# Optimization experiments

Measured on AMD Instinct MI355X. Metric: run time of the kernel, lower is better.

## Reference

```python
import jax, jax.numpy as jnp
import numpy as np

N, C, R, P1, P2 = 8, 3, 8, 512, 512
EPS = 1e-10


def setup_inputs() -> dict:
    key = jax.random.key(0)
    k1, k2, k3, k4 = jax.random.split(key, 4)
    X = jax.random.uniform(k1, (N, C, P1, P2), dtype=jnp.float32)
    S = jax.random.uniform(k2, (C, R), dtype=jnp.float32)
    # mimic the learned-init normalization: unit-norm columns of S
    S = S / jnp.linalg.norm(S, axis=0, keepdims=True)
    gamma = jax.random.uniform(k3, (1,), dtype=jnp.float32) * 1e-5
    lam = jax.random.uniform(k4, (1,), dtype=jnp.float32) * 1e-5
    return {"X": X, "S": S, "gamma": gamma, "lam": lam, "n_iter": 3}


def reference(X, S, gamma, lam, n_iter):
    n, c, p1, p2 = X.shape
    r = S.shape[1]
    p = p1 * p2
    X = X.reshape(n, c, p)
    gamma = jnp.abs(gamma)  # (1,)
    lam = jnp.abs(lam)      # (1,)
    Dt = jnp.zeros((n, r, p), dtype=X.dtype)
    x0 = jnp.mean(X, axis=2, keepdims=True)
    for _ in range(n_iter):
        # ---- D update (proximal gradient) ----
        SDt = jnp.einsum('cr,nrp->ncp', S, Dt)                    # [n,c,p]
        x0 = jnp.mean(X + SDt, axis=2, keepdims=True)             # [n,c,1]
        tau_D = 1.0 / jnp.sum(S * S)                              # 1/||S||_F^2
        Dt = Dt - tau_D * (jnp.einsum('cr,ncp->nrp', S, SDt + X)
                           - jnp.einsum('cr,ncq->nrq', S, x0))
        S_nrm = jnp.linalg.norm(S, axis=0).reshape(1, r, 1)       # col L2 norms of S
        Dt = jax.nn.relu(Dt - lam * gamma * tau_D * S_nrm)        # L1 prox
        Dt_L2 = jnp.linalg.norm(Dt, axis=2, keepdims=True)        # [n,r,1]
        scl = jax.nn.relu(Dt_L2 - lam * tau_D * S_nrm)
        scl = scl / Dt_L2 + EPS                                   # faithful to source
        Dt = Dt * scl                                             # L2 (group) prox
        # ---- S update (proximal gradient) ----
        SDt = jnp.einsum('cr,nrp->ncp', S, Dt)
        x0 = jnp.mean(X + SDt, axis=2, keepdims=True)             # [n,c,1]
        Dt_sum = jnp.sum(Dt, axis=2, keepdims=True)               # [n,r,1]
        tau_S = 1.0 / jnp.mean(jnp.sum(Dt * Dt, axis=(1, 2)))     # 1/mean ||Dt_i||_F^2
        G = (jnp.einsum('ncp,nrp->ncr', SDt + X, Dt)
             - x0 @ jnp.swapaxes(Dt_sum, 1, 2))                   # [n,c,r]
        S_grad = S - tau_S * jnp.mean(G, axis=0)                  # [c,r]
        Dt_nrm = jnp.mean(gamma * jnp.sum(jnp.abs(Dt), axis=2, keepdims=True)
                          + jnp.linalg.norm(Dt, axis=2, keepdims=True), axis=0)  # [r,1]
        S_nrm2 = jnp.linalg.norm(S_grad, axis=0, keepdims=True)   # [1,r]
        scl_S = jax.nn.relu(S_nrm2 - lam * tau_S * Dt_nrm.T)
        scl_S = scl_S / (S_nrm2 + EPS)
        S = S_grad * scl_S
        # ---- unit-norm rescaling of S columns ----
        S_nrm3 = jnp.linalg.norm(S, axis=0, keepdims=True)        # [1,r]
        S = S / (S_nrm3 + EPS)
        Dt = Dt * (S_nrm3.reshape(1, r, 1) + EPS)
    return (x0, S, Dt.reshape(n, r, p1, p2))
```

## Files before the change

### kernel.cpp

```cpp
#include <hip/hip_runtime.h>
#include <math.h>

#define N_ 8
#define C_ 3
#define R_ 8
#define P_ 262144
#define EPS_ 1e-10f
#define INVP_ (1.0f / (float)P_)
#define NRED 68

#define WS_S      0
#define WS_GAMMA  24
#define WS_LAM    25
#define WS_TAUD   26
#define WS_ALPHA  32
#define WS_MEANX  96
#define WS_B      120
#define WS_THRESH 184
#define WS_RED    192
#define WS_END    736

__global__ void k_init(float* __restrict__ ws, const float* __restrict__ S_in,
                       const float* __restrict__ gamma, const float* __restrict__ lam) {
    int t = threadIdx.x;
    if (t < 24) ws[WS_S + t] = S_in[t];
    if (t == 24) ws[WS_GAMMA] = fabsf(gamma[0]);
    if (t == 25) ws[WS_LAM]   = fabsf(lam[0]);
    for (int i = WS_ALPHA + t; i < WS_END; i += (int)blockDim.x) ws[i] = 0.0f;
}

__global__ void k_meanX(const float* __restrict__ X, float* __restrict__ ws) {
    const int slice = blockIdx.y;
    const float4* Xv = (const float4*)(X + (size_t)slice * P_);
    int tid  = blockIdx.x * blockDim.x + threadIdx.x;
    int nthr = gridDim.x * blockDim.x;
    float s = 0.f;
    for (int i = tid; i < P_ / 4; i += nthr) {
        float4 v = Xv[i];
        s += v.x + v.y + v.z + v.w;
    }
    for (int off = 32; off; off >>= 1) s += __shfl_down(s, off);
    __shared__ float lds[4];
    int lane = threadIdx.x & 63, wv = threadIdx.x >> 6;
    if (lane == 0) lds[wv] = s;
    __syncthreads();
    if (threadIdx.x == 0) {
        float t = lds[0] + lds[1] + lds[2] + lds[3];
        atomicAdd(&ws[WS_MEANX + slice], t);
    }
}

__global__ __launch_bounds__(64) void k_preD(float* __restrict__ ws) {
    const int lane = threadIdx.x;
    const int r = lane & 7, n = lane >> 3;
    __shared__ float sS[C_][R_];
    __shared__ float sMx[N_][C_];
    if (lane < 24) {
        float v = ws[WS_MEANX + lane] * INVP_;
        ws[WS_MEANX + lane] = v;
        sMx[lane / C_][lane % C_] = v;
    }
    if (lane < 24) sS[lane / R_][lane % R_] = ws[WS_S + lane];
    const float gamma = ws[WS_GAMMA], lam = ws[WS_LAM];
    __syncthreads();
    float ss = 0.f;
    for (int c = 0; c < C_; ++c)
        for (int rr = 0; rr < R_; ++rr) ss += sS[c][rr] * sS[c][rr];
    float tauD = 1.0f / ss;
    if (lane == 0) ws[WS_TAUD] = tauD;
    if (n == 0) {
        float sn = sqrtf(sS[0][r]*sS[0][r] + sS[1][r]*sS[1][r] + sS[2][r]*sS[2][r]);
        ws[WS_THRESH + r] = lam * gamma * tauD * sn;
    }
    float b = 0.f;
    for (int c = 0; c < C_; ++c) b += sS[c][r] * sMx[n][c];
    ws[WS_B + lane] = b;
}

__global__ __launch_bounds__(256) void k_pass(const float* __restrict__ X,
                                              float* __restrict__ Dt,
                                              float* __restrict__ ws, int first) {
    const int n = blockIdx.y;
    float S[C_][R_], al[R_], bb[R_], th[R_];
#pragma unroll
    for (int c = 0; c < C_; ++c)
#pragma unroll
        for (int r = 0; r < R_; ++r) S[c][r] = ws[WS_S + c * R_ + r];
#pragma unroll
    for (int r = 0; r < R_; ++r) {
        al[r] = ws[WS_ALPHA + n * R_ + r];
        bb[r] = ws[WS_B + n * R_ + r];
        th[r] = ws[WS_THRESH + r];
    }
    const float tauD = ws[WS_TAUD];

    const float4* Xv = (const float4*)(X + (size_t)n * C_ * P_);
    float4* Dv = (float4*)(Dt + (size_t)n * R_ * P_);
    const int P4 = P_ / 4;

    float acc[NRED];
#pragma unroll
    for (int k = 0; k < NRED; ++k) acc[k] = 0.f;

    int tid  = blockIdx.x * blockDim.x + threadIdx.x;
    int nthr = gridDim.x * blockDim.x;
    for (int i = tid; i < P4; i += nthr) {
        float4 xq[C_];
#pragma unroll
        for (int c = 0; c < C_; ++c) xq[c] = Xv[(size_t)c * P4 + i];
        float4 dq[R_];
        if (!first) {
#pragma unroll
            for (int r = 0; r < R_; ++r) dq[r] = Dv[(size_t)r * P4 + i];
        }
        float4 wq[R_];
#pragma unroll
        for (int j = 0; j < 4; ++j) {
            float ts[C_];
#pragma unroll
            for (int c = 0; c < C_; ++c) ts[c] = ((const float*)&xq[c])[j];
            float v[R_];
#pragma unroll
            for (int r = 0; r < R_; ++r) {
                v[r] = first ? 0.f : al[r] * ((const float*)&dq[r])[j];
#pragma unroll
                for (int c = 0; c < C_; ++c) ts[c] += S[c][r] * v[r];
            }
#pragma unroll
            for (int r = 0; r < R_; ++r) {
                float g = S[0][r] * ts[0] + S[1][r] * ts[1] + S[2][r] * ts[2] - bb[r];
                float u = v[r] - tauD * g - th[r];
                ((float*)&wq[r])[j] = fmaxf(u, 0.f);
            }
        }
#pragma unroll
        for (int r = 0; r < R_; ++r) Dv[(size_t)r * P4 + i] = wq[r];
#pragma unroll
        for (int r = 0; r < R_; ++r)
            acc[r] += wq[r].x + wq[r].y + wq[r].z + wq[r].w;
#pragma unroll
        for (int r = 0; r < R_; ++r)
#pragma unroll
            for (int r2 = 0; r2 <= r; ++r2)
                acc[8 + (r * (r + 1)) / 2 + r2] +=
                    wq[r].x * wq[r2].x + wq[r].y * wq[r2].y + wq[r].z * wq[r2].z + wq[r].w * wq[r2].w;
#pragma unroll
        for (int c = 0; c < C_; ++c)
#pragma unroll
            for (int r = 0; r < R_; ++r)
                acc[44 + c * R_ + r] +=
                    xq[c].x * wq[r].x + xq[c].y * wq[r].y + xq[c].z * wq[r].z + xq[c].w * wq[r].w;
    }

    __shared__ float lds[4][NRED];
    int lane = threadIdx.x & 63, wv = threadIdx.x >> 6;
#pragma unroll
    for (int k = 0; k < NRED; ++k) {
        float s = acc[k];
        for (int off = 32; off; off >>= 1) s += __shfl_down(s, off);
        if (lane == 0) lds[wv][k] = s;
    }
    __syncthreads();
    if (threadIdx.x < NRED) {
        float s = lds[0][threadIdx.x] + lds[1][threadIdx.x] + lds[2][threadIdx.x] + lds[3][threadIdx.x];
        atomicAdd(&ws[WS_RED + n * NRED + threadIdx.x], s);
    }
}

__global__ __launch_bounds__(64) void k_post(float* __restrict__ ws, float* __restrict__ out) {
    const int lane = threadIdx.x;
    const int r = lane & 7, n = lane >> 3;
    __shared__ float sS[C_][R_];
    __shared__ float sMx[N_][C_];
    __shared__ float sSumD[N_][R_];
    __shared__ float sGm[N_][R_][R_ + 1];
    __shared__ float sXd[N_][C_][R_];
    __shared__ float sScl[N_][R_];
    __shared__ float sX0[N_][C_];
    __shared__ float sSf[C_][R_];
    __shared__ float sAl[N_][R_];

    const float gamma = ws[WS_GAMMA], lam = ws[WS_LAM], tauD = ws[WS_TAUD];

    if (lane < 24) sS[lane / R_][lane % R_] = ws[WS_S + lane];
    if (lane < 24) sMx[lane / C_][lane % C_] = ws[WS_MEANX + lane];
    const float* red = ws + WS_RED + n * NRED;
    const float sumD = red[r];
    sSumD[n][r] = sumD;
#pragma unroll
    for (int r2 = 0; r2 < R_; ++r2) {
        int hi = r > r2 ? r : r2, lo = r + r2 - hi;
        sGm[n][r][r2] = red[8 + (hi * (hi + 1)) / 2 + lo];
    }
#pragma unroll
    for (int c = 0; c < C_; ++c) sXd[n][c][r] = red[44 + c * R_ + r];
    __syncthreads();

    const float snrm = sqrtf(sS[0][r]*sS[0][r] + sS[1][r]*sS[1][r] + sS[2][r]*sS[2][r]);
    const float Gdiag = sGm[n][r][r];
    const float L2 = sqrtf(Gdiag);
    const float sc = fmaxf(L2 - lam * tauD * snrm, 0.f) / L2 + EPS_;
    sScl[n][r] = sc;
    float ssq = sc * sc * Gdiag;
#pragma unroll
    for (int m = 1; m < 64; m <<= 1) ssq += __shfl_xor(ssq, m);
    float dtn = gamma * sc * sumD + sc * L2;
#pragma unroll
    for (int m = 8; m < 64; m <<= 1) dtn += __shfl_xor(dtn, m);
    __syncthreads();

    if (lane < N_ * C_) {
        int n2 = lane / C_, c2 = lane % C_;
        float x0 = sMx[n2][c2];
#pragma unroll
        for (int rr = 0; rr < R_; ++rr)
            x0 += sS[c2][rr] * sScl[n2][rr] * sSumD[n2][rr] * INVP_;
        sX0[n2][c2] = x0;
        out[lane] = x0;
    }
    __syncthreads();

    float Gc[C_];
#pragma unroll
    for (int c = 0; c < C_; ++c) {
        float t = 0.f;
#pragma unroll
        for (int r2 = 0; r2 < R_; ++r2)
            t += sS[c][r2] * sScl[n][r2] * sGm[n][r2][r];
        float G = t * sc + sc * sXd[n][c][r] - sX0[n][c] * sc * sumD;
#pragma unroll
        for (int m = 8; m < 64; m <<= 1) G += __shfl_xor(G, m);
        Gc[c] = G;
    }
    const float tauS = (float)N_ / ssq;
    float Sg[C_];
#pragma unroll
    for (int c = 0; c < C_; ++c) Sg[c] = sS[c][r] - tauS * (Gc[c] / (float)N_);
    const float sn2 = sqrtf(Sg[0]*Sg[0] + Sg[1]*Sg[1] + Sg[2]*Sg[2]);
    const float Dn = dtn / (float)N_;
    const float ssS = fmaxf(sn2 - lam * tauS * Dn, 0.f) / (sn2 + EPS_);
    float s1[C_];
#pragma unroll
    for (int c = 0; c < C_; ++c) s1[c] = Sg[c] * ssS;
    const float sn3 = sqrtf(s1[0]*s1[0] + s1[1]*s1[1] + s1[2]*s1[2]);
    float Sf[C_];
#pragma unroll
    for (int c = 0; c < C_; ++c) Sf[c] = s1[c] / (sn3 + EPS_);
    const float alpha = sc * (sn3 + EPS_);
    ws[WS_ALPHA + lane] = alpha;
    sAl[n][r] = alpha;
    if (n == 0) {
#pragma unroll
        for (int c = 0; c < C_; ++c) {
            ws[WS_S + c * R_ + r] = Sf[c];
            out[24 + c * R_ + r] = Sf[c];
            sSf[c][r] = Sf[c];
        }
    }
    float p2 = Sf[0]*Sf[0] + Sf[1]*Sf[1] + Sf[2]*Sf[2];
#pragma unroll
    for (int m = 1; m < 8; m <<= 1) p2 += __shfl_xor(p2, m);
    const float tauD2 = 1.0f / p2;
    if (lane == 0) ws[WS_TAUD] = tauD2;
    if (n == 0) {
        float snf = sqrtf(Sf[0]*Sf[0] + Sf[1]*Sf[1] + Sf[2]*Sf[2]);
        ws[WS_THRESH + r] = lam * gamma * tauD2 * snf;
    }
    __syncthreads();

    float b = 0.f;
#pragma unroll
    for (int c = 0; c < C_; ++c) {
        float x0n = sMx[n][c];
#pragma unroll
        for (int rr = 0; rr < R_; ++rr)
            x0n += sSf[c][rr] * sAl[n][rr] * sSumD[n][rr] * INVP_;
        b += sSf[c][r] * x0n;
    }
    ws[WS_B + lane] = b;
    for (int i = lane; i < N_ * NRED; i += 64) ws[WS_RED + i] = 0.f;
}

__global__ __launch_bounds__(256) void k_final(float* __restrict__ Dt, const float* __restrict__ ws) {
    const int nr = blockIdx.y;
    const float a = ws[WS_ALPHA + nr];
    float4* Dv = (float4*)(Dt + (size_t)nr * P_);
    int tid  = blockIdx.x * blockDim.x + threadIdx.x;
    int nthr = gridDim.x * blockDim.x;
    for (int i = tid; i < P_ / 4; i += nthr) {
        float4 v = Dv[i];
        v.x *= a; v.y *= a; v.z *= a; v.w *= a;
        Dv[i] = v;
    }
}

extern "C" void kernel_launch(void* const* d_in, const int* in_sizes, int n_in,
                              void* d_out, int out_size, void* d_ws, size_t ws_size,
                              hipStream_t stream) {
    const float* X     = (const float*)d_in[0];
    const float* S_in  = (const float*)d_in[1];
    const float* gamma = (const float*)d_in[2];
    const float* lam   = (const float*)d_in[3];

    float* out = (float*)d_out;
    float* ws  = (float*)d_ws;
    float* Dt  = out + 48;

    k_init<<<1, 256, 0, stream>>>(ws, S_in, gamma, lam);
    k_meanX<<<dim3(64, N_ * C_), 256, 0, stream>>>(X, ws);
    k_preD<<<1, 64, 0, stream>>>(ws);
    for (int it = 0; it < 3; ++it) {
        k_pass<<<dim3(64, N_), 256, 0, stream>>>(X, Dt, ws, it == 0 ? 1 : 0);
        k_post<<<1, 64, 0, stream>>>(ws, out);
    }
    k_final<<<dim3(64, N_ * R_), 256, 0, stream>>>(Dt, ws);
}
```

Before: 243.2 us.

## Fuse post-step into pass prologue and store intermediate Dt as bf16

Removes the single-block k_init, k_preD and k_post kernels by having every block of the next pass redundantly recompute the small S/tau/threshold update in an LDS prologue. Partial sums are stored per iteration so no zeroing pass is needed between kernels. When the workspace is large enough, intermediate Dt is kept in bf16 to halve the read/write traffic of the per-pixel passes. Rounding Dt to bf16 across iterations adds numerical error, and every block now repeats the serial prologue work.

```diff
diff --git a/kernel.cpp b/kernel.cpp
--- a/kernel.cpp
+++ b/kernel.cpp
@@ -5,292 +5,373 @@
 #define C_ 3
 #define R_ 8
 #define P_ 262144
+#define P4_ 65536
 #define EPS_ 1e-10f
 #define INVP_ (1.0f / (float)P_)
 #define NRED 68
 
-#define WS_S      0
-#define WS_GAMMA  24
-#define WS_LAM    25
-#define WS_TAUD   26
-#define WS_ALPHA  32
-#define WS_MEANX  96
-#define WS_B      120
-#define WS_THRESH 184
-#define WS_RED    192
-#define WS_END    736
-
-__global__ void k_init(float* __restrict__ ws, const float* __restrict__ S_in,
-                       const float* __restrict__ gamma, const float* __restrict__ lam) {
-    int t = threadIdx.x;
-    if (t < 24) ws[WS_S + t] = S_in[t];
-    if (t == 24) ws[WS_GAMMA] = fabsf(gamma[0]);
-    if (t == 25) ws[WS_LAM]   = fabsf(lam[0]);
-    for (int i = WS_ALPHA + t; i < WS_END; i += (int)blockDim.x) ws[i] = 0.0f;
-}
-
-__global__ void k_meanX(const float* __restrict__ X, float* __restrict__ ws) {
+#define WS_MXP 0
+#define WS_RED 1536
+#define WS_SL1 3200
+#define WS_SL2 3232
+#define WS_DTB 4096
+#define WS_NEED_BYTES ((size_t)16384 + (size_t)N_ * R_ * P_ * 2)
+
+struct PostLds {
+    float sS[C_][R_];
+    float sMx[N_][C_];
+    float sTh[R_];
+    float sB[N_][R_];
+    float sAl[N_][R_];
+    float sSumD[N_][R_];
+    float sGm[N_][R_][R_ + 1];
+    float sXd[N_][C_][R_];
+    float sScl[N_][R_];
+    float sX0[N_][C_];
+    float sTau[1];
+};
+
+__device__ __forceinline__ float bf2f(unsigned short s) {
+    return __uint_as_float(((unsigned)s) << 16);
+}
+__device__ __forceinline__ unsigned short f2bf(float f, float* back) {
+    unsigned u = __float_as_uint(f);
+    unsigned r = (u + 0x7FFFu + ((u >> 16) & 1u)) & 0xFFFF0000u;
+    *back = __uint_as_float(r);
+    return (unsigned short)(r >> 16);
+}
+
+__device__ void prologue(PostLds& L, int it, int blk0,
+                         const float* __restrict__ S_in,
+                         const float* __restrict__ gammap,
+                         const float* __restrict__ lamp,
+                         float* __restrict__ out, float* __restrict__ ws)
+{
+    const int t = threadIdx.x;
+    const int r_l = t & 7, n_l = (t >> 3) & 7;
+    const float gamma = fabsf(gammap[0]);
+    const float lam   = fabsf(lamp[0]);
+
+    if (t < 24) {
+        float s = 0.f;
+#pragma unroll
+        for (int b = 0; b < 64; ++b) s += ws[WS_MXP + t * 64 + b];
+        L.sMx[t / C_][t % C_] = s * INVP_;
+    }
+    if (t < 24)
+        L.sS[t / R_][t % R_] = (it <= 1) ? S_in[t]
+                              : (it == 2 ? ws[WS_SL1 + t] : ws[WS_SL2 + t]);
+    __syncthreads();
+
+    if (it == 0) {
+        float ss = 0.f;
+#pragma unroll
+        for (int c = 0; c < C_; ++c)
+#pragma unroll
+            for (int rr = 0; rr < R_; ++rr) ss += L.sS[c][rr] * L.sS[c][rr];
+        const float tauD0 = 1.f / ss;
+        if (t == 0) L.sTau[0] = tauD0;
+        if (t < R_) {
+            float sn = sqrtf(L.sS[0][t]*L.sS[0][t] + L.sS[1][t]*L.sS[1][t] + L.sS[2][t]*L.sS[2][t]);
+            L.sTh[t] = lam * gamma * tauD0 * sn;
+        }
+        if (t < 64) {
+            float b = 0.f;
+#pragma unroll
+            for (int c = 0; c < C_; ++c) b += L.sS[c][r_l] * L.sMx[n_l][c];
+            L.sB[n_l][r_l] = b;
+            L.sAl[n_l][r_l] = 0.f;
+        }
+        __syncthreads();
+        return;
+    }
+
+    float ssp = 0.f;
+#pragma unroll
+    for (int c = 0; c < C_; ++c)
+#pragma unroll
+        for (int rr = 0; rr < R_; ++rr) ssp += L.sS[c][rr] * L.sS[c][rr];
+    const float tauDc = 1.f / ssp;
+
+    if (t < 64) {
+        const float* red = ws + WS_RED + (size_t)((it - 1) * N_ + n_l) * NRED;
+        L.sSumD[n_l][r_l] = red[r_l];
+#pragma unroll
+        for (int r2 = 0; r2 < R_; ++r2) {
+            int hi = r_l > r2 ? r_l : r2, lo = r_l + r2 - hi;
+            L.sGm[n_l][r_l][r2] = red[8 + (hi * (hi + 1)) / 2 + lo];
+        }
+#pragma unroll
+        for (int c = 0; c < C_; ++c) L.sXd[n_l][c][r_l] = red[44 + c * R_ + r_l];
+    }
+    __syncthreads();
+
+    float sc = 0.f, ssq = 0.f, dtn = 0.f, sumD = 0.f;
+    if (t < 64) {
+        sumD = L.sSumD[n_l][r_l];
+        const float snrm = sqrtf(L.sS[0][r_l]*L.sS[0][r_l] + L.sS[1][r_l]*L.sS[1][r_l] + L.sS[2][r_l]*L.sS[2][r_l]);
+        const float Gdiag = L.sGm[n_l][r_l][r_l];
+        const float L2 = sqrtf(Gdiag);
+        sc = fmaxf(L2 - lam * tauDc * snrm, 0.f) / L2 + EPS_;
+        L.sScl[n_l][r_l] = sc;
+        ssq = sc * sc * Gdiag;
+#pragma unroll
+        for (int m = 1; m < 64; m <<= 1) ssq += __shfl_xor(ssq, m);
+        dtn = gamma * sc * sumD + sc * L2;
+#pragma unroll
+        for (int m = 8; m < 64; m <<= 1) dtn += __shfl_xor(dtn, m);
+    }
+    __syncthreads();
+
+    if (t < N_ * C_) {
+        int n2 = t / C_, c2 = t % C_;
+        float x0 = L.sMx[n2][c2];
+#pragma unroll
+        for (int rr = 0; rr < R_; ++rr)
+            x0 += L.sS[c2][rr] * L.sScl[n2][rr] * L.sSumD[n2][rr] * INVP_;
+        L.sX0[n2][c2] = x0;
+        if (it == 3 && blk0) out[t] = x0;
+    }
+    __syncthreads();
+
+    float Sf[C_] = {0.f, 0.f, 0.f};
+    float alpha = 0.f, tauDn = 0.f;
+    if (t < 64) {
+        float Gc[C_];
+#pragma unroll
+        for (int c = 0; c < C_; ++c) {
+            float tt = 0.f;
+#pragma unroll
+            for (int r2 = 0; r2 < R_; ++r2)
+                tt += L.sS[c][r2] * L.sScl[n_l][r2] * L.sGm[n_l][r2][r_l];
+            float G = tt * sc + sc * L.sXd[n_l][c][r_l] - L.sX0[n_l][c] * sc * sumD;
+#pragma unroll
+            for (int m = 8; m < 64; m <<= 1) G += __shfl_xor(G, m);
+            Gc[c] = G;
+        }
+        const float tauS = (float)N_ / ssq;
+        float Sg[C_];
+#pragma unroll
+        for (int c = 0; c < C_; ++c) Sg[c] = L.sS[c][r_l] - tauS * (Gc[c] / (float)N_);
+        const float sn2 = sqrtf(Sg[0]*Sg[0] + Sg[1]*Sg[1] + Sg[2]*Sg[2]);
+        const float Dn = dtn / (float)N_;
+        const float ssS = fmaxf(sn2 - lam * tauS * Dn, 0.f) / (sn2 + EPS_);
+        float s1[C_];
+#pragma unroll
+        for (int c = 0; c < C_; ++c) s1[c] = Sg[c] * ssS;
+        const float sn3 = sqrtf(s1[0]*s1[0] + s1[1]*s1[1] + s1[2]*s1[2]);
+#pragma unroll
+        for (int c = 0; c < C_; ++c) Sf[c] = s1[c] / (sn3 + EPS_);
+        alpha = sc * (sn3 + EPS_);
+        float p2 = Sf[0]*Sf[0] + Sf[1]*Sf[1] + Sf[2]*Sf[2];
+#pragma unroll
+        for (int m = 1; m < 8; m <<= 1) p2 += __shfl_xor(p2, m);
+        tauDn = 1.f / p2;
+    }
+    __syncthreads();
+    if (t < 64) {
+        L.sAl[n_l][r_l] = alpha;
+        if (n_l == 0) {
+#pragma unroll
+            for (int c = 0; c < C_; ++c) {
+                L.sS[c][r_l] = Sf[c];
+                if (it == 3 && blk0) out[24 + c * R_ + r_l] = Sf[c];
+            }
+            const float snf = sqrtf(Sf[0]*Sf[0] + Sf[1]*Sf[1] + Sf[2]*Sf[2]);
+            L.sTh[r_l] = lam * gamma * tauDn * snf;
+        }
+        if (t == 0) L.sTau[0] = tauDn;
+    }
+    __syncthreads();
+    if (t < 64) {
+        float b = 0.f;
+#pragma unroll
+        for (int c = 0; c < C_; ++c) {
+            float x0n = L.sMx[n_l][c];
+#pragma unroll
+            for (int rr = 0; rr < R_; ++rr)
+                x0n += L.sS[c][rr] * L.sAl[n_l][rr] * L.sSumD[n_l][rr] * INVP_;
+            b += L.sS[c][r_l] * x0n;
+        }
+        L.sB[n_l][r_l] = b;
+    }
+    if (blk0 && t < 24 && it < 3)
+        ws[(it == 1 ? WS_SL1 : WS_SL2) + t] = L.sS[t / R_][t % R_];
+    __syncthreads();
+}
+
+__global__ __launch_bounds__(256) void k_meanX(const float* __restrict__ X,
+                                               float* __restrict__ ws) {
     const int slice = blockIdx.y;
+    const int bx = blockIdx.x;
+    const int t = threadIdx.x;
+    const int flat = slice * 64 + bx;
+    if (flat < 7) {
+        int idx = flat * 256 + t;
+        if (idx < 3 * N_ * NRED) ws[WS_RED + idx] = 0.f;
+    }
     const float4* Xv = (const float4*)(X + (size_t)slice * P_);
-    int tid  = blockIdx.x * blockDim.x + threadIdx.x;
-    int nthr = gridDim.x * blockDim.x;
+    int tid = bx * 256 + t, nthr = 64 * 256;
     float s = 0.f;
-    for (int i = tid; i < P_ / 4; i += nthr) {
+    for (int i = tid; i < P4_; i += nthr) {
         float4 v = Xv[i];
         s += v.x + v.y + v.z + v.w;
     }
     for (int off = 32; off; off >>= 1) s += __shfl_down(s, off);
     __shared__ float lds[4];
-    int lane = threadIdx.x & 63, wv = threadIdx.x >> 6;
+    int lane = t & 63, wv = t >> 6;
     if (lane == 0) lds[wv] = s;
     __syncthreads();
-    if (threadIdx.x == 0) {
-        float t = lds[0] + lds[1] + lds[2] + lds[3];
-        atomicAdd(&ws[WS_MEANX + slice], t);
-    }
-}
-
-__global__ __launch_bounds__(64) void k_preD(float* __restrict__ ws) {
-    const int lane = threadIdx.x;
-    const int r = lane & 7, n = lane >> 3;
-    __shared__ float sS[C_][R_];
-    __shared__ float sMx[N_][C_];
-    if (lane < 24) {
-        float v = ws[WS_MEANX + lane] * INVP_;
-        ws[WS_MEANX + lane] = v;
-        sMx[lane / C_][lane % C_] = v;
-    }
-    if (lane < 24) sS[lane / R_][lane % R_] = ws[WS_S + lane];
-    const float gamma = ws[WS_GAMMA], lam = ws[WS_LAM];
-    __syncthreads();
-    float ss = 0.f;
+    if (t == 0) ws[WS_MXP + slice * 64 + bx] = lds[0] + lds[1] + lds[2] + lds[3];
+}
+
+template <bool BF16>
+__global__ __launch_bounds__(256, 1) void k_pass(
+    const float* __restrict__ X, const float* __restrict__ S_in,
+    const float* __restrict__ gammap, const float* __restrict__ lamp,
+    float* __restrict__ out, float* __restrict__ ws, int it)
+{
+    __shared__ PostLds L;
+    __shared__ float redLds[4][NRED];
+    const int t = threadIdx.x, n = blockIdx.y, bx = blockIdx.x;
+    prologue(L, it, (bx == 0 && n == 0) ? 1 : 0, S_in, gammap, lamp, out, ws);
+
+    float Sreg[C_][R_], al[R_], cst[R_];
+    const float tauD = L.sTau[0];
+#pragma unroll
     for (int c = 0; c < C_; ++c)
-        for (int rr = 0; rr < R_; ++rr) ss += sS[c][rr] * sS[c][rr];
-    float tauD = 1.0f / ss;
-    if (lane == 0) ws[WS_TAUD] = tauD;
-    if (n == 0) {
-        float sn = sqrtf(sS[0][r]*sS[0][r] + sS[1][r]*sS[1][r] + sS[2][r]*sS[2][r]);
-        ws[WS_THRESH + r] = lam * gamma * tauD * sn;
-    }
-    float b = 0.f;
-    for (int c = 0; c < C_; ++c) b += sS[c][r] * sMx[n][c];
-    ws[WS_B + lane] = b;
-}
-
-__global__ __launch_bounds__(256) void k_pass(const float* __restrict__ X,
-                                              float* __restrict__ Dt,
-                                              float* __restrict__ ws, int first) {
-    const int n = blockIdx.y;
-    float S[C_][R_], al[R_], bb[R_], th[R_];
-#pragma unroll
-    for (int c = 0; c < C_; ++c)
-#pragma unroll
-        for (int r = 0; r < R_; ++r) S[c][r] = ws[WS_S + c * R_ + r];
+#pragma unroll
+        for (int r = 0; r < R_; ++r) Sreg[c][r] = L.sS[c][r];
 #pragma unroll
     for (int r = 0; r < R_; ++r) {
-        al[r] = ws[WS_ALPHA + n * R_ + r];
-        bb[r] = ws[WS_B + n * R_ + r];
-        th[r] = ws[WS_THRESH + r];
-    }
-    const float tauD = ws[WS_TAUD];
+        al[r]  = L.sAl[n][r];
+        cst[r] = tauD * L.sB[n][r] - L.sTh[r];
+    }
 
     const float4* Xv = (const float4*)(X + (size_t)n * C_ * P_);
-    float4* Dv = (float4*)(Dt + (size_t)n * R_ * P_);
-    const int P4 = P_ / 4;
+    ushort4* Db = (ushort4*)((unsigned short*)(ws + WS_DTB));
+    float4*  Df = (float4*)(out + 48);
 
     float acc[NRED];
 #pragma unroll
     for (int k = 0; k < NRED; ++k) acc[k] = 0.f;
 
-    int tid  = blockIdx.x * blockDim.x + threadIdx.x;
-    int nthr = gridDim.x * blockDim.x;
-    for (int i = tid; i < P4; i += nthr) {
-        float4 xq[C_];
-#pragma unroll
-        for (int c = 0; c < C_; ++c) xq[c] = Xv[(size_t)c * P4 + i];
-        float4 dq[R_];
-        if (!first) {
-#pragma unroll
-            for (int r = 0; r < R_; ++r) dq[r] = Dv[(size_t)r * P4 + i];
-        }
-        float4 wq[R_];
-#pragma unroll
-        for (int j = 0; j < 4; ++j) {
-            float ts[C_];
-#pragma unroll
-            for (int c = 0; c < C_; ++c) ts[c] = ((const float*)&xq[c])[j];
+    const int tid = bx * 256 + t, nthr = 64 * 256;
+    for (int i = tid; i < P4_; i += nthr) {
+        float xa[C_][4];
+#pragma unroll
+        for (int c = 0; c < C_; ++c) {
+            float4 v = Xv[(size_t)c * P4_ + i];
+            xa[c][0] = v.x; xa[c][1] = v.y; xa[c][2] = v.z; xa[c][3] = v.w;
+        }
+        float dv[R_][4];
+        if (it > 0) {
+#pragma unroll
+            for (int r = 0; r < R_; ++r) {
+                if (BF16) {
+                    ushort4 d = Db[(size_t)(n * R_ + r) * P4_ + i];
+                    dv[r][0] = bf2f(d.x); dv[r][1] = bf2f(d.y);
+                    dv[r][2] = bf2f(d.z); dv[r][3] = bf2f(d.w);
+                } else {
+                    float4 d = Df[(size_t)(n * R_ + r) * P4_ + i];
+                    dv[r][0] = d.x; dv[r][1] = d.y; dv[r][2] = d.z; dv[r][3] = d.w;
+                }
+            }
+        }
+#pragma unroll
+        for (int q = 0; q < 4; ++q) {
+            float ts0 = xa[0][q], ts1 = xa[1][q], ts2 = xa[2][q];
             float v[R_];
 #pragma unroll
             for (int r = 0; r < R_; ++r) {
-                v[r] = first ? 0.f : al[r] * ((const float*)&dq[r])[j];
-#pragma unroll
-                for (int c = 0; c < C_; ++c) ts[c] += S[c][r] * v[r];
+                v[r] = (it > 0) ? al[r] * dv[r][q] : 0.f;
+                ts0 += Sreg[0][r] * v[r];
+                ts1 += Sreg[1][r] * v[r];
+                ts2 += Sreg[2][r] * v[r];
             }
 #pragma unroll
             for (int r = 0; r < R_; ++r) {
-                float g = S[0][r] * ts[0] + S[1][r] * ts[1] + S[2][r] * ts[2] - bb[r];
-                float u = v[r] - tauD * g - th[r];
-                ((float*)&wq[r])[j] = fmaxf(u, 0.f);
-            }
-        }
-#pragma unroll
-        for (int r = 0; r < R_; ++r) Dv[(size_t)r * P4 + i] = wq[r];
+                float sg = Sreg[0][r]*ts0 + Sreg[1][r]*ts1 + Sreg[2][r]*ts2;
+                float u = v[r] - tauD * sg + cst[r];
+                dv[r][q] = fmaxf(u, 0.f);
+            }
+        }
+#pragma unroll
+        for (int r = 0; r < R_; ++r) {
+            if (BF16) {
+                ushort4 o;
+                o.x = f2bf(dv[r][0], &dv[r][0]);
+                o.y = f2bf(dv[r][1], &dv[r][1]);
+                o.z = f2bf(dv[r][2], &dv[r][2]);
+                o.w = f2bf(dv[r][3], &dv[r][3]);
+                Db[(size_t)(n * R_ + r) * P4_ + i] = o;
+            } else {
+                float4 o;
+                o.x = dv[r][0]; o.y = dv[r][1]; o.z = dv[r][2]; o.w = dv[r][3];
+                Df[(size_t)(n * R_ + r) * P4_ + i] = o;
+            }
+        }
 #pragma unroll
         for (int r = 0; r < R_; ++r)
-            acc[r] += wq[r].x + wq[r].y + wq[r].z + wq[r].w;
+            acc[r] += dv[r][0] + dv[r][1] + dv[r][2] + dv[r][3];
 #pragma unroll
         for (int r = 0; r < R_; ++r)
 #pragma unroll
             for (int r2 = 0; r2 <= r; ++r2)
                 acc[8 + (r * (r + 1)) / 2 + r2] +=
-                    wq[r].x * wq[r2].x + wq[r].y * wq[r2].y + wq[r].z * wq[r2].z + wq[r].w * wq[r2].w;
+                    dv[r][0]*dv[r2][0] + dv[r][1]*dv[r2][1] + dv[r][2]*dv[r2][2] + dv[r][3]*dv[r2][3];
 #pragma unroll
         for (int c = 0; c < C_; ++c)
 #pragma unroll
             for (int r = 0; r < R_; ++r)
                 acc[44 + c * R_ + r] +=
-                    xq[c].x * wq[r].x + xq[c].y * wq[r].y + xq[c].z * wq[r].z + xq[c].w * wq[r].w;
-    }
-
-    __shared__ float lds[4][NRED];
-    int lane = threadIdx.x & 63, wv = threadIdx.x >> 6;
+                    xa[c][0]*dv[r][0] + xa[c][1]*dv[r][1] + xa[c][2]*dv[r][2] + xa[c][3]*dv[r][3];
+    }
+
+    const int lane = t & 63, wv = t >> 6;
 #pragma unroll
     for (int k = 0; k < NRED; ++k) {
         float s = acc[k];
         for (int off = 32; off; off >>= 1) s += __shfl_down(s, off);
-        if (lane == 0) lds[wv][k] = s;
-    }
-    __syncthreads();
-    if (threadIdx.x < NRED) {
-        float s = lds[0][threadIdx.x] + lds[1][threadIdx.x] + lds[2][threadIdx.x] + lds[3][threadIdx.x];
-        atomicAdd(&ws[WS_RED + n * NRED + threadIdx.x], s);
-    }
-}
-
-__global__ __launch_bounds__(64) void k_post(float* __restrict__ ws, float* __restrict__ out) {
-    const int lane = threadIdx.x;
-    const int r = lane & 7, n = lane >> 3;
-    __shared__ float sS[C_][R_];
-    __shared__ float sMx[N_][C_];
-    __shared__ float sSumD[N_][R_];
-    __shared__ float sGm[N_][R_][R_ + 1];
-    __shared__ float sXd[N_][C_][R_];
-    __shared__ float sScl[N_][R_];
-    __shared__ float sX0[N_][C_];
-    __shared__ float sSf[C_][R_];
-    __shared__ float sAl[N_][R_];
-
-    const float gamma = ws[WS_GAMMA], lam = ws[WS_LAM], tauD = ws[WS_TAUD];
-
-    if (lane < 24) sS[lane / R_][lane % R_] = ws[WS_S + lane];
-    if (lane < 24) sMx[lane / C_][lane % C_] = ws[WS_MEANX + lane];
-    const float* red = ws + WS_RED + n * NRED;
-    const float sumD = red[r];
-    sSumD[n][r] = sumD;
-#pragma unroll
-    for (int r2 = 0; r2 < R_; ++r2) {
-        int hi = r > r2 ? r : r2, lo = r + r2 - hi;
-        sGm[n][r][r2] = red[8 + (hi * (hi + 1)) / 2 + lo];
-    }
-#pragma unroll
-    for (int c = 0; c < C_; ++c) sXd[n][c][r] = red[44 + c * R_ + r];
-    __syncthreads();
-
-    const float snrm = sqrtf(sS[0][r]*sS[0][r] + sS[1][r]*sS[1][r] + sS[2][r]*sS[2][r]);
-    const float Gdiag = sGm[n][r][r];
-    const float L2 = sqrtf(Gdiag);
-    const float sc = fmaxf(L2 - lam * tauD * snrm, 0.f) / L2 + EPS_;
-    sScl[n][r] = sc;
-    float ssq = sc * sc * Gdiag;
-#pragma unroll
-    for (int m = 1; m < 64; m <<= 1) ssq += __shfl_xor(ssq, m);
-    float dtn = gamma * sc * sumD + sc * L2;
-#pragma unroll
-    for (int m = 8; m < 64; m <<= 1) dtn += __shfl_xor(dtn, m);
-    __syncthreads();
-
-    if (lane < N_ * C_) {
-        int n2 = lane / C_, c2 = lane % C_;
-        float x0 = sMx[n2][c2];
-#pragma unroll
-        for (int rr = 0; rr < R_; ++rr)
-            x0 += sS[c2][rr] * sScl[n2][rr] * sSumD[n2][rr] * INVP_;
-        sX0[n2][c2] = x0;
-        out[lane] = x0;
-    }
-    __syncthreads();
-
-    float Gc[C_];
-#pragma unroll
-    for (int c = 0; c < C_; ++c) {
-        float t = 0.f;
-#pragma unroll
-        for (int r2 = 0; r2 < R_; ++r2)
-            t += sS[c][r2] * sScl[n][r2] * sGm[n][r2][r];
-        float G = t * sc + sc * sXd[n][c][r] - sX0[n][c] * sc * sumD;
-#pragma unroll
-        for (int m = 8; m < 64; m <<= 1) G += __shfl_xor(G, m);
-        Gc[c] = G;
-    }
-    const float tauS = (float)N_ / ssq;
-    float Sg[C_];
-#pragma unroll
-    for (int c = 0; c < C_; ++c) Sg[c] = sS[c][r] - tauS * (Gc[c] / (float)N_);
-    const float sn2 = sqrtf(Sg[0]*Sg[0] + Sg[1]*Sg[1] + Sg[2]*Sg[2]);
-    const float Dn = dtn / (float)N_;
-    const float ssS = fmaxf(sn2 - lam * tauS * Dn, 0.f) / (sn2 + EPS_);
-    float s1[C_];
-#pragma unroll
-    for (int c = 0; c < C_; ++c) s1[c] = Sg[c] * ssS;
-    const float sn3 = sqrtf(s1[0]*s1[0] + s1[1]*s1[1] + s1[2]*s1[2]);
-    float Sf[C_];
-#pragma unroll
-    for (int c = 0; c < C_; ++c) Sf[c] = s1[c] / (sn3 + EPS_);
-    const float alpha = sc * (sn3 + EPS_);
-    ws[WS_ALPHA + lane] = alpha;
-    sAl[n][r] = alpha;
-    if (n == 0) {
-#pragma unroll
-        for (int c = 0; c < C_; ++c) {
-            ws[WS_S + c * R_ + r] = Sf[c];
-            out[24 + c * R_ + r] = Sf[c];
-            sSf[c][r] = Sf[c];
-        }
-    }
-    float p2 = Sf[0]*Sf[0] + Sf[1]*Sf[1] + Sf[2]*Sf[2];
-#pragma unroll
-    for (int m = 1; m < 8; m <<= 1) p2 += __shfl_xor(p2, m);
-    const float tauD2 = 1.0f / p2;
-    if (lane == 0) ws[WS_TAUD] = tauD2;
-    if (n == 0) {
-        float snf = sqrtf(Sf[0]*Sf[0] + Sf[1]*Sf[1] + Sf[2]*Sf[2]);
-        ws[WS_THRESH + r] = lam * gamma * tauD2 * snf;
-    }
-    __syncthreads();
-
-    float b = 0.f;
-#pragma unroll
-    for (int c = 0; c < C_; ++c) {
-        float x0n = sMx[n][c];
-#pragma unroll
-        for (int rr = 0; rr < R_; ++rr)
-            x0n += sSf[c][rr] * sAl[n][rr] * sSumD[n][rr] * INVP_;
-        b += sSf[c][r] * x0n;
-    }
-    ws[WS_B + lane] = b;
-    for (int i = lane; i < N_ * NRED; i += 64) ws[WS_RED + i] = 0.f;
-}
-
-__global__ __launch_bounds__(256) void k_final(float* __restrict__ Dt, const float* __restrict__ ws) {
-    const int nr = blockIdx.y;
-    const float a = ws[WS_ALPHA + nr];
-    float4* Dv = (float4*)(Dt + (size_t)nr * P_);
-    int tid  = blockIdx.x * blockDim.x + threadIdx.x;
-    int nthr = gridDim.x * blockDim.x;
-    for (int i = tid; i < P_ / 4; i += nthr) {
-        float4 v = Dv[i];
-        v.x *= a; v.y *= a; v.z *= a; v.w *= a;
-        Dv[i] = v;
+        if (lane == 0) redLds[wv][k] = s;
+    }
+    __syncthreads();
+    if (t < NRED)
+        atomicAdd(ws + WS_RED + (size_t)(it * N_ + n) * NRED + t,
+                  redLds[0][t] + redLds[1][t] + redLds[2][t] + redLds[3][t]);
+}
+
+template <bool BF16>
+__global__ __launch_bounds__(256, 1) void k_final(
+    const float* __restrict__ S_in, const float* __restrict__ gammap,
+    const float* __restrict__ lamp, float* __restrict__ out, float* __restrict__ ws)
+{
+    __shared__ PostLds L;
+    const int t = threadIdx.x, n = blockIdx.y, bx = blockIdx.x;
+    prologue(L, 3, (bx == 0 && n == 0) ? 1 : 0, S_in, gammap, lamp, out, ws);
+
+    float alv[R_];
+#pragma unroll
+    for (int r = 0; r < R_; ++r) alv[r] = L.sAl[n][r];
+
+    const ushort4* Db = (const ushort4*)((const unsigned short*)(ws + WS_DTB));
+    float4* Df = (float4*)(out + 48);
+    const int tid = bx * 256 + t, nthr = 64 * 256;
+    for (int i = tid; i < P4_; i += nthr) {
+#pragma unroll
+        for (int r = 0; r < R_; ++r) {
+            const float a = alv[r];
+            float4 o;
+            if (BF16) {
+                ushort4 d = Db[(size_t)(n * R_ + r) * P4_ + i];
+                o.x = bf2f(d.x) * a; o.y = bf2f(d.y) * a;
+                o.z = bf2f(d.z) * a; o.w = bf2f(d.w) * a;
+            } else {
+                float4 d = Df[(size_t)(n * R_ + r) * P4_ + i];
+                o.x = d.x * a; o.y = d.y * a; o.z = d.z * a; o.w = d.w * a;
+            }
+            Df[(size_t)(n * R_ + r) * P4_ + i] = o;
+        }
     }
 }
 
@@ -304,14 +385,18 @@
 
     float* out = (float*)d_out;
     float* ws  = (float*)d_ws;
-    float* Dt  = out + 48;
-
-    k_init<<<1, 256, 0, stream>>>(ws, S_in, gamma, lam);
-    k_meanX<<<dim3(64, N_ * C_), 256, 0, stream>>>(X, ws);
-    k_preD<<<1, 64, 0, stream>>>(ws);
+
+    const bool bf = (ws_size >= WS_NEED_BYTES);
+
+    k_meanX<<<dim3(64, 24), 256, 0, stream>>>(X, ws);
     for (int it = 0; it < 3; ++it) {
-        k_pass<<<dim3(64, N_), 256, 0, stream>>>(X, Dt, ws, it == 0 ? 1 : 0);
-        k_post<<<1, 64, 0, stream>>>(ws, out);
-    }
-    k_final<<<dim3(64, N_ * R_), 256, 0, stream>>>(Dt, ws);
-}
+        if (bf)
+            k_pass<true><<<dim3(64, N_), 256, 0, stream>>>(X, S_in, gamma, lam, out, ws, it);
+        else
+            k_pass<false><<<dim3(64, N_), 256, 0, stream>>>(X, S_in, gamma, lam, out, ws, it);
+    }
+    if (bf)
+        k_final<true><<<dim3(64, N_), 256, 0, stream>>>(S_in, gamma, lam, out, ws);
+    else
+        k_final<false><<<dim3(64, N_), 256, 0, stream>>>(S_in, gamma, lam, out, ws);
+}
```

Measured after the change: 216.7 us. 10.9% less time.
